# Kernel tuning notes

Measured on AMD Instinct MI355X. Metric: run time of the kernel, lower is better.

The kernel has to match this reference:

```python
import jax, jax.numpy as jnp
import numpy as np

LN_EPS = 1e-5

def _layernorm(x, g, b):
    mu = jnp.mean(x, axis=-1, keepdims=True)
    var = jnp.mean(jnp.square(x - mu), axis=-1, keepdims=True)
    return (x - mu) * jax.lax.rsqrt(var + LN_EPS) * g + b

def setup_inputs() -> dict:
    key = jax.random.key(0)
    ks = jax.random.split(key, 8)
    B, T, C = 4, 2048, 1024
    s = 0.02
    return {
        "x": jax.random.normal(ks[0], (B, T, C), jnp.float32),
        "w_qkv": jax.random.normal(ks[1], (C, 3 * C), jnp.float32) * s,
        "b_qkv": jnp.zeros((3 * C,), jnp.float32),
        "w_out": jax.random.normal(ks[2], (C, C), jnp.float32) * s,
        "b_out": jnp.zeros((C,), jnp.float32),
        "w1": jax.random.normal(ks[3], (C, 4 * C), jnp.float32) * s,
        "b1": jnp.zeros((4 * C,), jnp.float32),
        "w2": jax.random.normal(ks[4], (4 * C, C), jnp.float32) * s,
        "b2": jnp.zeros((C,), jnp.float32),
        "g1": jnp.ones((C,), jnp.float32),
        "be1": jnp.zeros((C,), jnp.float32),
        "g2": jnp.ones((C,), jnp.float32),
        "be2": jnp.zeros((C,), jnp.float32),
        "n_head": 16,
    }

def reference(x, w_qkv, b_qkv, w_out, b_out, w1, b1, w2, b2, g1, be1, g2, be2, n_head):
    B, T, C = x.shape
    H = n_head
    D = C // H
    # --- causal self-attention ---
    qkv = x @ w_qkv + b_qkv                      # [B,T,3C]
    q, k, v = jnp.split(qkv, 3, axis=-1)
    q = q.reshape(B, T, H, D).transpose(0, 2, 1, 3)  # [B,H,T,D]
    k = k.reshape(B, T, H, D).transpose(0, 2, 1, 3)
    v = v.reshape(B, T, H, D).transpose(0, 2, 1, 3)
    attn = jnp.einsum("bhqd,bhkd->bhqk", q, k) * (1.0 / np.sqrt(D))
    causal = jnp.tril(jnp.ones((T, T), bool))
    attn = jnp.where(causal, attn, jnp.float32(-jnp.inf))
    attn = jax.nn.softmax(attn, axis=-1)
    y = jnp.einsum("bhqk,bhkd->bhqd", attn, v)
    y = y.transpose(0, 2, 1, 3).reshape(B, T, C)
    y = y @ w_out + b_out
    # post-norm residual (norm applied to sublayer output)
    x = x + _layernorm(y, g1, be1)
    # --- MLP ---
    h = jax.nn.gelu(x @ w1 + b1, approximate=False)
    h = h @ w2 + b2
    x = x + _layernorm(h, g2, be2)
    return x
```

## Files before the change

### kernel.cpp

```cpp
#include <hip/hip_runtime.h>
#include <hip/hip_bf16.h>

typedef unsigned short ushort_t;
using bf16x8 = __attribute__((ext_vector_type(8))) short;
using f32x4  = __attribute__((ext_vector_type(4))) float;

#define DEV __device__ __forceinline__

DEV unsigned short f2bf(float f) {
    unsigned int u = __builtin_bit_cast(unsigned int, f);
    u = (u + 0x7fffu + ((u >> 16) & 1u)) >> 16;
    return (unsigned short)u;
}

DEV float bf2f(unsigned short s) {
    return __builtin_bit_cast(float, (unsigned int)s << 16);
}

DEV int cvtpk_bf16(float lo, float hi) {
    int r;
    asm("v_cvt_pk_bf16_f32 %0, %1, %2" : "=v"(r) : "v"(lo), "v"(hi));
    return r;
}

DEV void gload16(const unsigned short* g, unsigned short* l) {
    __builtin_amdgcn_global_load_lds(
        (const __attribute__((address_space(1))) void*)g,
        (__attribute__((address_space(3))) void*)l, 16, 0, 0);
}

DEV float gelu_f(float v) {
    float t = __builtin_amdgcn_exp2f(v * 2.4554946f);
    return v * t * __builtin_amdgcn_rcpf(t + 1.0f);
}

__global__ __launch_bounds__(256) void cvtbf_kernel(const float* __restrict__ in,
                                                    unsigned short* __restrict__ out) {
    int i = (blockIdx.x * 256 + threadIdx.x) * 4;
    float4 v = *(const float4*)&in[i];
    out[i + 0] = f2bf(v.x);
    out[i + 1] = f2bf(v.y);
    out[i + 2] = f2bf(v.z);
    out[i + 3] = f2bf(v.w);
}

__global__ __launch_bounds__(256) void transpose_cvt_kernel(const float* __restrict__ in,
                                                            unsigned short* __restrict__ out,
                                                            int R, int C) {
    __shared__ float t[32][33];
    int tx = threadIdx.x, ty = threadIdx.y;
    int c0 = blockIdx.x * 32, r0 = blockIdx.y * 32;
#pragma unroll
    for (int i = 0; i < 4; ++i)
        t[ty + i * 8][tx] = in[(size_t)(r0 + ty + i * 8) * C + c0 + tx];
    __syncthreads();
#pragma unroll
    for (int i = 0; i < 4; ++i)
        out[(size_t)(c0 + ty + i * 8) * R + r0 + tx] = f2bf(t[tx][ty + i * 8]);
}

__global__ __launch_bounds__(256) void vtrans_kernel(const unsigned short* __restrict__ qkvb,
                                                     unsigned short* __restrict__ vtg) {
    __shared__ unsigned short t[64 * 66];
    const int tid = threadIdx.x;
    const int t0 = blockIdx.x * 64;
    const int bh = blockIdx.y;
    const int b = bh >> 4, h = bh & 15;
    const unsigned short* src = qkvb + (size_t)(b * 2048 + t0) * 3072 + 2048 + h * 64;
#pragma unroll
    for (int c = 0; c < 2; ++c) {
        int cid = c * 256 + tid;
        int row = cid >> 3, cc = cid & 7;
        *(int4*)&t[row * 66 + cc * 8] = *(const int4*)&src[(size_t)row * 3072 + cc * 8];
    }
    __syncthreads();
    unsigned short* dst = vtg + (size_t)bh * 64 * 2048 + t0;
#pragma unroll
    for (int c = 0; c < 2; ++c) {
        int cid = c * 256 + tid;
        int d = cid >> 3, cc2 = cid & 7;
        bf16x8 v;
#pragma unroll
        for (int j = 0; j < 8; ++j) v[j] = (short)t[(cc2 * 8 + j) * 66 + d];
        *(bf16x8*)&dst[(size_t)d * 2048 + cc2 * 8] = v;
    }
}

template <int ACT, int OBF, int OBF2>
__global__ __launch_bounds__(512, 2) void gemm256_kernel(
    const unsigned short* __restrict__ A, const unsigned short* __restrict__ Bt,
    const float* __restrict__ bias, void* __restrict__ out, void* __restrict__ out2,
    int N, int Ktot, int gridNt, int GM, int nSlices) {
    __shared__ __align__(16) unsigned short lA[2][256 * 64];
    __shared__ __align__(16) unsigned short lB[2][256 * 64];
    const int tid = threadIdx.x;
    const int lane = tid & 63, wid = tid >> 6;
    const int g = lane >> 4, lr = lane & 15;
    const int wm = wid >> 2, wn = wid & 3;

    const int nwg = gridDim.x, cpx = nwg >> 3, bid = blockIdx.x;
    const int wkid = (bid & 7) * cpx + (bid >> 3);
    const int bps = nwg / nSlices;
    const int sl = wkid / bps, rem = wkid % bps;
    const int mt = (rem / (GM * gridNt)) * GM + (rem % GM);
    const int nt = (rem / GM) % gridNt;
    const int m0 = mt * 256, n0 = nt * 256;
    const int Ksl = Ktot / nSlices;
    const int kb0 = sl * Ksl;
    const int nkt = Ksl >> 6;
    void* outp = (sl == 0) ? out : out2;

    auto stageA = [&](int s, int kt, int bb) {
        int c = s * 512 + tid;
        int row = c & 255, kb = c >> 8;
        gload16(&A[(size_t)(m0 + row) * Ktot + kb0 + kt * 64 + kb * 8],
                &lA[bb][(size_t)(s * 512 + (tid & ~63)) * 8]);
    };
    auto stageB = [&](int s, int kt, int bb) {
        int c = s * 512 + tid;
        int row = c & 255, kb = c >> 8;
        gload16(&Bt[(size_t)(n0 + row) * Ktot + kb0 + kt * 64 + kb * 8],
                &lB[bb][(size_t)(s * 512 + (tid & ~63)) * 8]);
    };

    f32x4 acc[8][4] = {};
    bf16x8 bfr[4];

    stageA(0, 0, 0); stageA(1, 0, 0); stageB(0, 0, 0); stageB(1, 0, 0);
    stageA(2, 0, 0); stageA(3, 0, 0); stageB(2, 0, 0); stageB(3, 0, 0);
    asm volatile("s_waitcnt vmcnt(4)" ::: "memory");
    __builtin_amdgcn_s_barrier();
    asm volatile("" ::: "memory");

    for (int kt = 0; kt < nkt; ++kt) {
        const int buf = kt & 1;
        const bool more = (kt + 1 < nkt);
#pragma unroll
        for (int p = 0; p < 4; ++p) {
            const int ks = p >> 1, mh = p & 1;
            bf16x8 af[4];
#pragma unroll
            for (int mf2 = 0; mf2 < 4; ++mf2) {
                int c = (ks * 4 + g) * 256 + wm * 128 + (mh * 4 + mf2) * 16 + lr;
                af[mf2] = *(const bf16x8*)&lA[buf][(size_t)c * 8];
            }
            if (mh == 0) {
#pragma unroll
                for (int nf = 0; nf < 4; ++nf) {
                    int c = (ks * 4 + g) * 256 + wn * 64 + nf * 16 + lr;
                    bfr[nf] = *(const bf16x8*)&lB[buf][(size_t)c * 8];
                }
            }
            if (more) {
                if (p == 0)      { stageA(0, kt + 1, buf ^ 1); stageA(1, kt + 1, buf ^ 1); }
                else if (p == 1) { stageB(0, kt + 1, buf ^ 1); stageB(1, kt + 1, buf ^ 1); }
                else if (p == 2) { stageA(2, kt + 1, buf ^ 1); stageA(3, kt + 1, buf ^ 1); }
                else             { stageB(2, kt + 1, buf ^ 1); stageB(3, kt + 1, buf ^ 1); }
            }
            __builtin_amdgcn_s_barrier();
            asm volatile("s_waitcnt lgkmcnt(0)" ::: "memory");
            __builtin_amdgcn_sched_barrier(0);
            __builtin_amdgcn_s_setprio(1);
#pragma unroll
            for (int mf2 = 0; mf2 < 4; ++mf2)
#pragma unroll
                for (int nf = 0; nf < 4; ++nf)
                    acc[mh * 4 + mf2][nf] = __builtin_amdgcn_mfma_f32_16x16x32_bf16(
                        af[mf2], bfr[nf], acc[mh * 4 + mf2][nf], 0, 0, 0);
            __builtin_amdgcn_s_setprio(0);
            __builtin_amdgcn_sched_barrier(0);
            if (p == 1) {
                if (more) asm volatile("s_waitcnt vmcnt(4)" ::: "memory");
                else      asm volatile("s_waitcnt vmcnt(0)" ::: "memory");
            } else if (p == 3) {
                if (more) asm volatile("s_waitcnt vmcnt(4)" ::: "memory");
            }
            __builtin_amdgcn_s_barrier();
            asm volatile("" ::: "memory");
        }
    }

#pragma unroll
    for (int mf = 0; mf < 8; ++mf) {
#pragma unroll
        for (int nf = 0; nf < 4; ++nf) {
            int col = n0 + wn * 64 + nf * 16 + lr;
            float bv = (sl == 0) ? bias[col] : 0.0f;
#pragma unroll
            for (int r = 0; r < 4; ++r) {
                int row = m0 + wm * 128 + mf * 16 + g * 4 + r;
                float v = acc[mf][nf][r] + bv;
                if (ACT == 1) v = gelu_f(v);
                if (sl == 0) {
                    if (OBF)
                        ((unsigned short*)outp)[(size_t)row * N + col] = f2bf(v);
                    else
                        ((float*)outp)[(size_t)row * N + col] = v;
                } else {
                    if (OBF2)
                        ((unsigned short*)outp)[(size_t)row * N + col] = f2bf(v);
                    else
                        ((float*)outp)[(size_t)row * N + col] = v;
                }
            }
        }
    }
}

__global__ __launch_bounds__(256, 2) void attn_kernel(const unsigned short* __restrict__ qkv,
                                                      const unsigned short* __restrict__ vtg,
                                                      unsigned short* __restrict__ y) {
    __shared__ unsigned short Kl[2][128 * 64];
    __shared__ unsigned short Vl[2][64 * 128];
    const int tid = threadIdx.x, lane = tid & 63, w = tid >> 6;
    const int g = lane >> 4, lr = lane & 15;
    const int id = blockIdx.x + 8 * (blockIdx.y + 16 * blockIdx.z);
    const int xcd = id & 7, wrk = id >> 3;
    const int bh = xcd * 8 + (wrk & 7);
    const int p = wrk >> 3;
    const int b = bh >> 4, h = bh & 15;
    const size_t rs3 = 3072;
    const unsigned short* qbase = qkv + (size_t)b * 2048 * rs3 + h * 64;
    const unsigned short* kbase = qbase + 1024;
    const unsigned short* vbase = vtg + (size_t)bh * 64 * 2048;

    int ksoff[4], vsoff[4], ldoff[4];
#pragma unroll
    for (int c = 0; c < 4; ++c) {
        int cid = c * 256 + tid;
        int krow = cid >> 3, kcc = cid & 7;
        ksoff[c] = krow * 3072 + (kcc ^ (krow & 7) ^ ((krow >> 3) & 7)) * 8;
        int d = cid >> 4, tcs = cid & 15;
        vsoff[c] = d * 2048 + (tcs ^ ((d & 7) ^ ((d >> 3) & 7))) * 8;
        ldoff[c] = (c * 256 + (tid & ~63)) * 8;
    }

    const int idxP0 = 4 * (32 * (g & 1) + lr);
    const int idxP1 = idxP0 + 64;
    int idxA[4];
#pragma unroll
    for (int r = 0; r < 4; ++r) idxA[r] = 4 * (g * 20 + r);
    const bool ghigh = (g >> 1) != 0;
    const float qscale = 0.125f * 1.44269504089f;

    auto process = [&](int J) {
        const int q0w = J * 128 + w * 32;
        const int ktend = J + 1;
#pragma unroll
        for (int c = 0; c < 4; ++c) {
            gload16(&kbase[ksoff[c]], &Kl[0][ldoff[c]]);
            gload16(&vbase[vsoff[c]], &Vl[0][ldoff[c]]);
        }
        int qf[2][2][4];
#pragma unroll
        for (int sub = 0; sub < 2; ++sub)
#pragma unroll
            for (int f = 0; f < 2; ++f) {
                int4 v = *(const int4*)&qbase[(size_t)(q0w + sub * 16 + lr) * rs3 + f * 32 + g * 8];
                int vv[4] = {v.x, v.y, v.z, v.w};
#pragma unroll
                for (int i = 0; i < 4; ++i) {
                    unsigned int u = (unsigned int)vv[i];
                    float lo = __builtin_bit_cast(float, u << 16) * qscale;
                    float hi = __builtin_bit_cast(float, u & 0xffff0000u) * qscale;
                    qf[sub][f][i] = cvtpk_bf16(lo, hi);
                }
            }

        f32x4 O[2][4] = {};
        float m_[2] = {-3.0e38f, -3.0e38f}, l_[2] = {0.f, 0.f};

        int buf = 0;
        for (int kt = 0; kt < ktend; ++kt) {
            asm volatile("s_waitcnt vmcnt(0)" ::: "memory");
            __builtin_amdgcn_s_barrier();
            asm volatile("" ::: "memory");
            if (kt + 1 < ktend) {
#pragma unroll
                for (int c = 0; c < 4; ++c) {
                    gload16(&kbase[(size_t)(kt + 1) * 128 * 3072 + ksoff[c]], &Kl[buf ^ 1][ldoff[c]]);
                    gload16(&vbase[vsoff[c] + (kt + 1) * 128], &Vl[buf ^ 1][ldoff[c]]);
                }
            }
            const unsigned short* Kc = Kl[buf];
            const unsigned short* Vc = Vl[buf];

            f32x4 s0[8], s1[8];
#pragma unroll
            for (int st = 0; st < 8; ++st) {
                int rbase = (st * 16 + lr) * 64;
                int sw = (lr & 7) ^ ((st * 2 + (lr >> 3)) & 7);
                bf16x8 kf0 = *(const bf16x8*)&Kc[rbase + ((g ^ sw) * 8)];
                bf16x8 kf1 = *(const bf16x8*)&Kc[rbase + (((4 + g) ^ sw) * 8)];
                f32x4 a = {};
                a = __builtin_amdgcn_mfma_f32_16x16x32_bf16(kf0, *(const bf16x8*)&qf[0][0], a, 0, 0, 0);
                a = __builtin_amdgcn_mfma_f32_16x16x32_bf16(kf1, *(const bf16x8*)&qf[0][1], a, 0, 0, 0);
                s0[st] = a;
                f32x4 c = {};
                c = __builtin_amdgcn_mfma_f32_16x16x32_bf16(kf0, *(const bf16x8*)&qf[1][0], c, 0, 0, 0);
                c = __builtin_amdgcn_mfma_f32_16x16x32_bf16(kf1, *(const bf16x8*)&qf[1][1], c, 0, 0, 0);
                s1[st] = c;
            }

            int wt0[4][4], wt1[4][4];
#pragma unroll
            for (int sub = 0; sub < 2; ++sub) {
                f32x4* s = (sub == 0) ? s0 : s1;
                const int qmin = q0w + sub * 16;
                if (kt == J) {
                    int qv = qmin + lr;
#pragma unroll
                    for (int st = 0; st < 8; ++st) {
                        int keyb = kt * 128 + st * 16 + g * 4;
#pragma unroll
                        for (int r = 0; r < 4; ++r)
                            if (keyb + r > qv) s[st][r] = -3.0e38f;
                    }
                }
                float mx = fmaxf(fmaxf(s[0][0], s[0][1]), fmaxf(s[0][2], s[0][3]));
#pragma unroll
                for (int st = 1; st < 8; ++st)
                    mx = fmaxf(mx, fmaxf(fmaxf(s[st][0], s[st][1]), fmaxf(s[st][2], s[st][3])));
                mx = fmaxf(mx, __shfl_xor(mx, 16));
                mx = fmaxf(mx, __shfl_xor(mx, 32));
                if (__any(mx - m_[sub] > 11.5f)) {
                    float mnew = fmaxf(m_[sub], mx);
                    float alpha = __builtin_amdgcn_exp2f(m_[sub] - mnew);
                    m_[sub] = mnew;
                    l_[sub] *= alpha;
                    int av = __builtin_bit_cast(int, alpha);
                    f32x4* Os = O[sub];
#pragma unroll
                    for (int r = 0; r < 4; ++r) {
                        float ar = __builtin_bit_cast(float, __builtin_amdgcn_ds_bpermute(idxA[r], av));
#pragma unroll
                        for (int dt = 0; dt < 4; ++dt) Os[dt][r] *= ar;
                    }
                }
                float rs = 0.f;
#pragma unroll
                for (int st = 0; st < 8; ++st)
#pragma unroll
                    for (int r = 0; r < 4; ++r) {
                        float pp = __builtin_amdgcn_exp2f(s[st][r] - m_[sub]);
                        s[st][r] = pp;
                        rs += pp;
                    }
                rs += __shfl_xor(rs, 16);
                rs += __shfl_xor(rs, 32);
                l_[sub] += rs;
                int ws_[8][2];
#pragma unroll
                for (int st = 0; st < 8; ++st) {
                    ws_[st][0] = cvtpk_bf16(s[st][0], s[st][1]);
                    ws_[st][1] = cvtpk_bf16(s[st][2], s[st][3]);
                }
                int(*wt)[4] = (sub == 0) ? wt0 : wt1;
#pragma unroll
                for (int ks = 0; ks < 4; ++ks)
#pragma unroll
                    for (int hp = 0; hp < 4; ++hp) {
                        int idx = (hp < 2) ? idxP0 : idxP1;
                        int v0 = __builtin_amdgcn_ds_bpermute(idx, ws_[2 * ks][hp & 1]);
                        int v1 = __builtin_amdgcn_ds_bpermute(idx, ws_[2 * ks + 1][hp & 1]);
                        wt[ks][hp] = ghigh ? v1 : v0;
                    }
            }

#pragma unroll
            for (int ks = 0; ks < 4; ++ks) {
                bf16x8 pa0 = *(const bf16x8*)&wt0[ks][0];
                bf16x8 pa1 = *(const bf16x8*)&wt1[ks][0];
#pragma unroll
                for (int dt = 0; dt < 4; ++dt) {
                    int d = dt * 16 + lr;
                    int tc = (ks * 4 + g) ^ ((lr & 7) ^ ((dt * 2 + (lr >> 3)) & 7));
                    bf16x8 vf = *(const bf16x8*)&Vc[d * 128 + tc * 8];
                    O[0][dt] = __builtin_amdgcn_mfma_f32_16x16x32_bf16(pa0, vf, O[0][dt], 0, 0, 0);
                    O[1][dt] = __builtin_amdgcn_mfma_f32_16x16x32_bf16(pa1, vf, O[1][dt], 0, 0, 0);
                }
            }
            buf ^= 1;
        }

#pragma unroll
        for (int sub = 0; sub < 2; ++sub) {
            int lv = __builtin_bit_cast(int, l_[sub]);
#pragma unroll
            for (int r = 0; r < 4; ++r) {
                float lval = __builtin_bit_cast(float, __builtin_amdgcn_ds_bpermute(idxA[r], lv));
                float inv = __builtin_amdgcn_rcpf(lval);
                int q = q0w + sub * 16 + g * 4 + r;
#pragma unroll
                for (int dt = 0; dt < 4; ++dt)
                    y[(size_t)(b * 2048 + q) * 1024 + h * 64 + dt * 16 + lr] =
                        f2bf(O[sub][dt][r] * inv);
            }
        }
    };

    process(15 - p);
    __syncthreads();
    process(p);
}

template <int WRITE_BF, int D2BF>
__global__ __launch_bounds__(256) void ln_kernel(const float* __restrict__ base,
                                                 const float* __restrict__ delta,
                                                 const void* __restrict__ delta2,
                                                 const float* __restrict__ gw,
                                                 const float* __restrict__ bw,
                                                 float* __restrict__ outf,
                                                 unsigned short* __restrict__ outb) {
    const int row = blockIdx.x;
    const int tid = threadIdx.x;
    const float* d = delta + (size_t)row * 1024;
    const float* bs = base + (size_t)row * 1024;
    float4 x = *(const float4*)&d[tid * 4];
    if (D2BF) {
        const unsigned short* d2 = (const unsigned short*)delta2 + (size_t)row * 1024 + tid * 4;
        ushort4 u = *(const ushort4*)d2;
        x.x += bf2f(u.x); x.y += bf2f(u.y); x.z += bf2f(u.z); x.w += bf2f(u.w);
    } else {
        const float* d2 = (const float*)delta2 + (size_t)row * 1024 + tid * 4;
        float4 x2 = *(const float4*)d2;
        x.x += x2.x; x.y += x2.y; x.z += x2.z; x.w += x2.w;
    }
    float s = x.x + x.y + x.z + x.w;
    float s2 = x.x * x.x + x.y * x.y + x.z * x.z + x.w * x.w;
#pragma unroll
    for (int off = 1; off < 64; off <<= 1) {
        s += __shfl_xor(s, off);
        s2 += __shfl_xor(s2, off);
    }
    __shared__ float red[8];
    if ((tid & 63) == 0) {
        red[tid >> 6] = s;
        red[4 + (tid >> 6)] = s2;
    }
    __syncthreads();
    s = red[0] + red[1] + red[2] + red[3];
    s2 = red[4] + red[5] + red[6] + red[7];
    float mu = s * (1.f / 1024.f);
    float var = s2 * (1.f / 1024.f) - mu * mu;
    float rsig = rsqrtf(var + 1e-5f);
    float4 bb = *(const float4*)&bs[tid * 4];
    float4 gv = *(const float4*)&gw[tid * 4];
    float4 bv = *(const float4*)&bw[tid * 4];
    float4 o;
    o.x = bb.x + (x.x - mu) * rsig * gv.x + bv.x;
    o.y = bb.y + (x.y - mu) * rsig * gv.y + bv.y;
    o.z = bb.z + (x.z - mu) * rsig * gv.z + bv.z;
    o.w = bb.w + (x.w - mu) * rsig * gv.w + bv.w;
    *(float4*)&outf[(size_t)row * 1024 + tid * 4] = o;
    if (WRITE_BF) {
        unsigned short* ob = outb + (size_t)row * 1024 + tid * 4;
        ob[0] = f2bf(o.x);
        ob[1] = f2bf(o.y);
        ob[2] = f2bf(o.z);
        ob[3] = f2bf(o.w);
    }
}

extern "C" void kernel_launch(void* const* d_in, const int* in_sizes, int n_in,
                              void* d_out, int out_size, void* d_ws, size_t ws_size,
                              hipStream_t stream) {
    const float* x = (const float*)d_in[0];
    const float* w_qkv = (const float*)d_in[1];
    const float* b_qkv = (const float*)d_in[2];
    const float* w_out = (const float*)d_in[3];
    const float* b_out = (const float*)d_in[4];
    const float* w1 = (const float*)d_in[5];
    const float* b1 = (const float*)d_in[6];
    const float* w2 = (const float*)d_in[7];
    const float* b2 = (const float*)d_in[8];
    const float* g1 = (const float*)d_in[9];
    const float* be1 = (const float*)d_in[10];
    const float* g2 = (const float*)d_in[11];
    const float* be2 = (const float*)d_in[12];

    const size_t MB = 1ull << 20;
    if (ws_size < 184 * MB) return;
    char* ws = (char*)d_ws;
    unsigned short* xb    = (unsigned short*)(ws + 0);
    unsigned short* vtg   = (unsigned short*)(ws + 0);
    float*          attnp1= (float*)(ws + 0);
    unsigned short* hb    = (unsigned short*)(ws + 0);
    unsigned short* wqkvt = (unsigned short*)(ws + 16 * MB);
    unsigned short* qkvb  = (unsigned short*)(ws + 22 * MB);
    unsigned short* woutt = (unsigned short*)(ws + 70 * MB);
    unsigned short* yb    = (unsigned short*)(ws + 72 * MB);
    unsigned short* ff1b  = (unsigned short*)(ws + 72 * MB);
    float*          attnp = (float*)(ws + 88 * MB);
    float*          ff    = (float*)(ws + 88 * MB);
    float*          x2f   = (float*)(ws + 120 * MB);
    unsigned short* x2b   = (unsigned short*)(ws + 152 * MB);
    unsigned short* w1t   = (unsigned short*)(ws + 168 * MB);
    unsigned short* w2t   = (unsigned short*)(ws + 176 * MB);

    cvtbf_kernel<<<8192, 256, 0, stream>>>(x, xb);
    transpose_cvt_kernel<<<dim3(96, 32), dim3(32, 8), 0, stream>>>(w_qkv, wqkvt, 1024, 3072);
    transpose_cvt_kernel<<<dim3(32, 32), dim3(32, 8), 0, stream>>>(w_out, woutt, 1024, 1024);
    transpose_cvt_kernel<<<dim3(128, 32), dim3(32, 8), 0, stream>>>(w1, w1t, 1024, 4096);
    transpose_cvt_kernel<<<dim3(32, 128), dim3(32, 8), 0, stream>>>(w2, w2t, 4096, 1024);
    gemm256_kernel<0, 1, 1><<<384, 512, 0, stream>>>(xb, wqkvt, b_qkv, qkvb, nullptr,
                                                     3072, 1024, 12, 4, 1);
    vtrans_kernel<<<dim3(32, 64), 256, 0, stream>>>(qkvb, vtg);
    attn_kernel<<<dim3(8, 16, 4), 256, 0, stream>>>(qkvb, vtg, yb);
    gemm256_kernel<0, 0, 0><<<256, 512, 0, stream>>>(yb, woutt, b_out, attnp, attnp1,
                                                     1024, 1024, 4, 8, 2);
    ln_kernel<1, 0><<<8192, 256, 0, stream>>>(x, attnp, attnp1, g1, be1, x2f, x2b);
    gemm256_kernel<1, 1, 1><<<512, 512, 0, stream>>>(x2b, w1t, b1, hb, nullptr,
                                                     4096, 1024, 16, 4, 1);
    gemm256_kernel<0, 0, 1><<<256, 512, 0, stream>>>(hb, w2t, b2, ff, ff1b,
                                                     1024, 4096, 4, 8, 2);
    ln_kernel<0, 1><<<8192, 256, 0, stream>>>(x2f, ff, ff1b, g2, be2, (float*)d_out, nullptr);
}
```

Before: 465.8 us.

## Shrink GEMM tiles to 256x128xK32 for higher occupancy; drop fp32 residual copy

Result: slower. 579.7 us (+24.5%).

```diff
diff --git a/kernel.cpp b/kernel.cpp
--- a/kernel.cpp
+++ b/kernel.cpp
@@ -87,12 +87,12 @@
 }
 
 template <int ACT, int OBF, int OBF2>
-__global__ __launch_bounds__(512, 2) void gemm256_kernel(
+__global__ __launch_bounds__(512, 4) void gemmw_kernel(
     const unsigned short* __restrict__ A, const unsigned short* __restrict__ Bt,
     const float* __restrict__ bias, void* __restrict__ out, void* __restrict__ out2,
     int N, int Ktot, int gridNt, int GM, int nSlices) {
-    __shared__ __align__(16) unsigned short lA[2][256 * 64];
-    __shared__ __align__(16) unsigned short lB[2][256 * 64];
+    __shared__ __align__(16) unsigned short lA[2][256 * 32];
+    __shared__ __align__(16) unsigned short lB[2][128 * 32];
     const int tid = threadIdx.x;
     const int lane = tid & 63, wid = tid >> 6;
     const int g = lane >> 4, lr = lane & 15;
@@ -104,87 +104,65 @@
     const int sl = wkid / bps, rem = wkid % bps;
     const int mt = (rem / (GM * gridNt)) * GM + (rem % GM);
     const int nt = (rem / GM) % gridNt;
-    const int m0 = mt * 256, n0 = nt * 256;
+    const int m0 = mt * 256, n0 = nt * 128;
     const int Ksl = Ktot / nSlices;
     const int kb0 = sl * Ksl;
-    const int nkt = Ksl >> 6;
+    const int nkt = Ksl >> 5;
     void* outp = (sl == 0) ? out : out2;
 
-    auto stageA = [&](int s, int kt, int bb) {
-        int c = s * 512 + tid;
-        int row = c & 255, kb = c >> 8;
-        gload16(&A[(size_t)(m0 + row) * Ktot + kb0 + kt * 64 + kb * 8],
-                &lA[bb][(size_t)(s * 512 + (tid & ~63)) * 8]);
+    auto stage = [&](int kt, int bb) {
+#pragma unroll
+        for (int s = 0; s < 2; ++s) {
+            int c = s * 512 + tid;
+            int row = c & 255, kb = c >> 8;
+            gload16(&A[(size_t)(m0 + row) * Ktot + kb0 + kt * 32 + kb * 8],
+                    &lA[bb][(size_t)(s * 512 + (tid & ~63)) * 8]);
+        }
+        {
+            int row = tid & 127, kb = tid >> 7;
+            gload16(&Bt[(size_t)(n0 + row) * Ktot + kb0 + kt * 32 + kb * 8],
+                    &lB[bb][(size_t)(tid & ~63) * 8]);
+        }
     };
-    auto stageB = [&](int s, int kt, int bb) {
-        int c = s * 512 + tid;
-        int row = c & 255, kb = c >> 8;
-        gload16(&Bt[(size_t)(n0 + row) * Ktot + kb0 + kt * 64 + kb * 8],
-                &lB[bb][(size_t)(s * 512 + (tid & ~63)) * 8]);
-    };
-
-    f32x4 acc[8][4] = {};
-    bf16x8 bfr[4];
-
-    stageA(0, 0, 0); stageA(1, 0, 0); stageB(0, 0, 0); stageB(1, 0, 0);
-    stageA(2, 0, 0); stageA(3, 0, 0); stageB(2, 0, 0); stageB(3, 0, 0);
-    asm volatile("s_waitcnt vmcnt(4)" ::: "memory");
-    __builtin_amdgcn_s_barrier();
-    asm volatile("" ::: "memory");
+
+    f32x4 acc[8][2] = {};
+
+    stage(0, 0);
 
     for (int kt = 0; kt < nkt; ++kt) {
         const int buf = kt & 1;
-        const bool more = (kt + 1 < nkt);
-#pragma unroll
-        for (int p = 0; p < 4; ++p) {
-            const int ks = p >> 1, mh = p & 1;
-            bf16x8 af[4];
-#pragma unroll
-            for (int mf2 = 0; mf2 < 4; ++mf2) {
-                int c = (ks * 4 + g) * 256 + wm * 128 + (mh * 4 + mf2) * 16 + lr;
-                af[mf2] = *(const bf16x8*)&lA[buf][(size_t)c * 8];
-            }
-            if (mh == 0) {
-#pragma unroll
-                for (int nf = 0; nf < 4; ++nf) {
-                    int c = (ks * 4 + g) * 256 + wn * 64 + nf * 16 + lr;
-                    bfr[nf] = *(const bf16x8*)&lB[buf][(size_t)c * 8];
-                }
-            }
-            if (more) {
-                if (p == 0)      { stageA(0, kt + 1, buf ^ 1); stageA(1, kt + 1, buf ^ 1); }
-                else if (p == 1) { stageB(0, kt + 1, buf ^ 1); stageB(1, kt + 1, buf ^ 1); }
-                else if (p == 2) { stageA(2, kt + 1, buf ^ 1); stageA(3, kt + 1, buf ^ 1); }
-                else             { stageB(2, kt + 1, buf ^ 1); stageB(3, kt + 1, buf ^ 1); }
-            }
-            __builtin_amdgcn_s_barrier();
-            asm volatile("s_waitcnt lgkmcnt(0)" ::: "memory");
-            __builtin_amdgcn_sched_barrier(0);
-            __builtin_amdgcn_s_setprio(1);
-#pragma unroll
-            for (int mf2 = 0; mf2 < 4; ++mf2)
-#pragma unroll
-                for (int nf = 0; nf < 4; ++nf)
-                    acc[mh * 4 + mf2][nf] = __builtin_amdgcn_mfma_f32_16x16x32_bf16(
-                        af[mf2], bfr[nf], acc[mh * 4 + mf2][nf], 0, 0, 0);
-            __builtin_amdgcn_s_setprio(0);
-            __builtin_amdgcn_sched_barrier(0);
-            if (p == 1) {
-                if (more) asm volatile("s_waitcnt vmcnt(4)" ::: "memory");
-                else      asm volatile("s_waitcnt vmcnt(0)" ::: "memory");
-            } else if (p == 3) {
-                if (more) asm volatile("s_waitcnt vmcnt(4)" ::: "memory");
-            }
-            __builtin_amdgcn_s_barrier();
-            asm volatile("" ::: "memory");
-        }
+        asm volatile("s_waitcnt vmcnt(0)" ::: "memory");
+        __builtin_amdgcn_s_barrier();
+        asm volatile("" ::: "memory");
+        if (kt + 1 < nkt) stage(kt + 1, buf ^ 1);
+        bf16x8 af[8], bfr[2];
+#pragma unroll
+        for (int mf = 0; mf < 8; ++mf) {
+            int ci = g * 256 + wm * 128 + mf * 16 + lr;
+            af[mf] = *(const bf16x8*)&lA[buf][(size_t)ci * 8];
+        }
+#pragma unroll
+        for (int nf = 0; nf < 2; ++nf) {
+            int ci = g * 128 + wn * 32 + nf * 16 + lr;
+            bfr[nf] = *(const bf16x8*)&lB[buf][(size_t)ci * 8];
+        }
+        asm volatile("s_waitcnt lgkmcnt(0)" ::: "memory");
+        __builtin_amdgcn_sched_barrier(0);
+        __builtin_amdgcn_s_setprio(1);
+#pragma unroll
+        for (int mf = 0; mf < 8; ++mf)
+#pragma unroll
+            for (int nf = 0; nf < 2; ++nf)
+                acc[mf][nf] = __builtin_amdgcn_mfma_f32_16x16x32_bf16(
+                    af[mf], bfr[nf], acc[mf][nf], 0, 0, 0);
+        __builtin_amdgcn_s_setprio(0);
     }
 
 #pragma unroll
     for (int mf = 0; mf < 8; ++mf) {
 #pragma unroll
-        for (int nf = 0; nf < 4; ++nf) {
-            int col = n0 + wn * 64 + nf * 16 + lr;
+        for (int nf = 0; nf < 2; ++nf) {
+            int col = n0 + wn * 32 + nf * 16 + lr;
             float bv = (sl == 0) ? bias[col] : 0.0f;
 #pragma unroll
             for (int r = 0; r < 4; ++r) {
@@ -404,8 +382,8 @@
     process(p);
 }
 
-template <int WRITE_BF, int D2BF>
-__global__ __launch_bounds__(256) void ln_kernel(const float* __restrict__ base,
+template <int WRITE_BF, int D2BF, int BASEBF>
+__global__ __launch_bounds__(256) void ln_kernel(const void* __restrict__ base,
                                                  const float* __restrict__ delta,
                                                  const void* __restrict__ delta2,
                                                  const float* __restrict__ gw,
@@ -415,7 +393,6 @@
     const int row = blockIdx.x;
     const int tid = threadIdx.x;
     const float* d = delta + (size_t)row * 1024;
-    const float* bs = base + (size_t)row * 1024;
     float4 x = *(const float4*)&d[tid * 4];
     if (D2BF) {
         const unsigned short* d2 = (const unsigned short*)delta2 + (size_t)row * 1024 + tid * 4;
@@ -444,7 +421,14 @@
     float mu = s * (1.f / 1024.f);
     float var = s2 * (1.f / 1024.f) - mu * mu;
     float rsig = rsqrtf(var + 1e-5f);
-    float4 bb = *(const float4*)&bs[tid * 4];
+    float4 bb;
+    if (BASEBF) {
+        const unsigned short* bs = (const unsigned short*)base + (size_t)row * 1024 + tid * 4;
+        ushort4 u = *(const ushort4*)bs;
+        bb.x = bf2f(u.x); bb.y = bf2f(u.y); bb.z = bf2f(u.z); bb.w = bf2f(u.w);
+    } else {
+        bb = *(const float4*)((const float*)base + (size_t)row * 1024 + tid * 4);
+    }
     float4 gv = *(const float4*)&gw[tid * 4];
     float4 bv = *(const float4*)&bw[tid * 4];
     float4 o;
@@ -452,7 +436,7 @@
     o.y = bb.y + (x.y - mu) * rsig * gv.y + bv.y;
     o.z = bb.z + (x.z - mu) * rsig * gv.z + bv.z;
     o.w = bb.w + (x.w - mu) * rsig * gv.w + bv.w;
-    *(float4*)&outf[(size_t)row * 1024 + tid * 4] = o;
+    if (outf) *(float4*)&outf[(size_t)row * 1024 + tid * 4] = o;
     if (WRITE_BF) {
         unsigned short* ob = outb + (size_t)row * 1024 + tid * 4;
         ob[0] = f2bf(o.x);
@@ -493,7 +477,6 @@
     unsigned short* ff1b  = (unsigned short*)(ws + 72 * MB);
     float*          attnp = (float*)(ws + 88 * MB);
     float*          ff    = (float*)(ws + 88 * MB);
-    float*          x2f   = (float*)(ws + 120 * MB);
     unsigned short* x2b   = (unsigned short*)(ws + 152 * MB);
     unsigned short* w1t   = (unsigned short*)(ws + 168 * MB);
     unsigned short* w2t   = (unsigned short*)(ws + 176 * MB);
@@ -503,16 +486,16 @@
     transpose_cvt_kernel<<<dim3(32, 32), dim3(32, 8), 0, stream>>>(w_out, woutt, 1024, 1024);
     transpose_cvt_kernel<<<dim3(128, 32), dim3(32, 8), 0, stream>>>(w1, w1t, 1024, 4096);
     transpose_cvt_kernel<<<dim3(32, 128), dim3(32, 8), 0, stream>>>(w2, w2t, 4096, 1024);
-    gemm256_kernel<0, 1, 1><<<384, 512, 0, stream>>>(xb, wqkvt, b_qkv, qkvb, nullptr,
-                                                     3072, 1024, 12, 4, 1);
+    gemmw_kernel<0, 1, 1><<<768, 512, 0, stream>>>(xb, wqkvt, b_qkv, qkvb, nullptr,
+                                                   3072, 1024, 24, 4, 1);
     vtrans_kernel<<<dim3(32, 64), 256, 0, stream>>>(qkvb, vtg);
     attn_kernel<<<dim3(8, 16, 4), 256, 0, stream>>>(qkvb, vtg, yb);
-    gemm256_kernel<0, 0, 0><<<256, 512, 0, stream>>>(yb, woutt, b_out, attnp, attnp1,
-                                                     1024, 1024, 4, 8, 2);
-    ln_kernel<1, 0><<<8192, 256, 0, stream>>>(x, attnp, attnp1, g1, be1, x2f, x2b);
-    gemm256_kernel<1, 1, 1><<<512, 512, 0, stream>>>(x2b, w1t, b1, hb, nullptr,
-                                                     4096, 1024, 16, 4, 1);
-    gemm256_kernel<0, 0, 1><<<256, 512, 0, stream>>>(hb, w2t, b2, ff, ff1b,
-                                                     1024, 4096, 4, 8, 2);
-    ln_kernel<0, 1><<<8192, 256, 0, stream>>>(x2f, ff, ff1b, g2, be2, (float*)d_out, nullptr);
-}
+    gemmw_kernel<0, 0, 0><<<512, 512, 0, stream>>>(yb, woutt, b_out, attnp, attnp1,
+                                                   1024, 1024, 8, 8, 2);
+    ln_kernel<1, 0, 0><<<8192, 256, 0, stream>>>(x, attnp, attnp1, g1, be1, nullptr, x2b);
+    gemmw_kernel<1, 1, 1><<<1024, 512, 0, stream>>>(x2b, w1t, b1, hb, nullptr,
+                                                    4096, 1024, 32, 4, 1);
+    gemmw_kernel<0, 0, 1><<<512, 512, 0, stream>>>(hb, w2t, b2, ff, ff1b,
+                                                   1024, 4096, 8, 8, 2);
+    ln_kernel<0, 1, 1><<<8192, 256, 0, stream>>>(x2b, ff, ff1b, g2, be2, (float*)d_out, nullptr);
+}
```
